# Performance work log

Hardware: AMD Instinct MI355X
Metric: run time of the kernel (lower is better)

## Reference

```python
import jax, jax.numpy as jnp
import numpy as np

N = 50000      # nodes
E = 800000     # edges (before self-loops)
IN = 256       # in_channels
HID = 16       # hidden_channels per head
HEADS = 8
OUT = 64       # out_channels (classes)
NEG_SLOPE = 0.2  # PyG GATConv leaky_relu slope


def setup_inputs() -> dict:
    key = jax.random.key(0)
    ks = jax.random.split(key, 10)
    x = jax.random.normal(ks[0], (N, IN), jnp.float32)
    edge_index = jax.random.randint(ks[1], (2, E), 0, N, dtype=jnp.int32)
    g = lambda k, shape: jax.random.normal(k, shape, jnp.float32) * (1.0 / np.sqrt(shape[0]))
    W1 = g(ks[2], (IN, HEADS * HID))
    a_src1 = jax.random.normal(ks[3], (HEADS, HID), jnp.float32) * 0.1
    a_dst1 = jax.random.normal(ks[4], (HEADS, HID), jnp.float32) * 0.1
    b1 = jnp.zeros((HEADS * HID,), jnp.float32)
    W2 = g(ks[5], (HEADS * HID, OUT))
    a_src2 = jax.random.normal(ks[6], (1, OUT), jnp.float32) * 0.1
    a_dst2 = jax.random.normal(ks[7], (1, OUT), jnp.float32) * 0.1
    b2 = jnp.zeros((OUT,), jnp.float32)
    return {"x": x, "edge_index": edge_index, "W1": W1, "a_src1": a_src1,
            "a_dst1": a_dst1, "b1": b1, "W2": W2, "a_src2": a_src2,
            "a_dst2": a_dst2, "b2": b2}


def gat_conv(x, src, dst, W, a_s, a_d, b, heads, concat):
    # x: [n, f]; edges src->dst; attention softmax over incoming edges of dst
    n = x.shape[0]
    h = (x @ W).reshape(n, heads, -1)                 # [n, H, d]
    al_s = jnp.einsum('nhd,hd->nh', h, a_s)           # [n, H]
    al_d = jnp.einsum('nhd,hd->nh', h, a_d)
    e = jax.nn.leaky_relu(al_s[src] + al_d[dst], negative_slope=NEG_SLOPE)  # [E, H]
    m = jax.ops.segment_max(e, dst, num_segments=n)   # stable scatter-softmax
    ex = jnp.exp(e - m[dst])
    den = jax.ops.segment_sum(ex, dst, num_segments=n)
    alpha = ex / (den[dst] + 1e-16)                   # [E, H]
    out = jax.ops.segment_sum(h[src] * alpha[:, :, None], dst, num_segments=n)  # [n, H, d]
    out = out.reshape(n, -1) if concat else out.mean(axis=1)
    return out + b


def reference(x, edge_index, W1, a_src1, a_dst1, b1, W2, a_src2, a_dst2, b2):
    # inference mode: dropout disabled. PyG GATConv adds self-loops by default.
    n = x.shape[0]
    loop = jnp.arange(n, dtype=edge_index.dtype)
    ei = jnp.concatenate([edge_index, jnp.stack([loop, loop])], axis=1)
    src, dst = ei[0], ei[1]
    h = gat_conv(x, src, dst, W1, a_src1, a_dst1, b1, HEADS, True)
    h = jax.nn.elu(h)
    h = gat_conv(h, src, dst, W2, a_src2, a_dst2, b2, 1, False)
    return jax.nn.log_softmax(h, axis=1)
```

## Files before the change

kernel.cpp:

```cpp
#include <hip/hip_runtime.h>
#include <hip/hip_bf16.h>


typedef __attribute__((ext_vector_type(8))) short short8;
typedef __attribute__((ext_vector_type(4))) float f4;
typedef __attribute__((ext_vector_type(2))) float float2v;

#define NCHUNK 64
#define NRANGE 4
#define RSIZE 16384
#define CONVB 80

#define A1PAD 72
#define B1PAD 264
#define G2PAD 136

__device__ __forceinline__ unsigned short f2bf(float f) {
  unsigned int u = __builtin_bit_cast(unsigned int, f);
  u += 0x7fffu + ((u >> 16) & 1u);
  return (unsigned short)(u >> 16);
}
__device__ __forceinline__ float bf2f(unsigned short h) {
  unsigned int u = ((unsigned int)h) << 16;
  return __builtin_bit_cast(float, u);
}

__device__ __forceinline__ unsigned char f2fp8(float f) {
  unsigned int u = __builtin_bit_cast(unsigned int, f);
  unsigned int s = (u >> 24) & 0x80u;
  float a = fabsf(f);
  a = fminf(a, 448.f);
  if (a < 0.015625f) {
    int m = (int)rintf(a * 512.f);
    return (unsigned char)(s | (unsigned)m);
  }
  unsigned int ub = __builtin_bit_cast(unsigned int, a);
  ub += 0xFFFFFu + ((ub >> 20) & 1u);
  unsigned int e = (ub >> 23) - 120u;
  unsigned int m = (ub >> 20) & 7u;
  if (e > 15u) { e = 15u; m = 6u; }
  return (unsigned char)(s | (e << 3) | m);
}

__global__ __launch_bounds__(512) void hist_kernel(const int* __restrict__ ei,
                                                   int* __restrict__ hist,
                                                   const float* __restrict__ W1,
                                                   const float* __restrict__ W2,
                                                   unsigned short* __restrict__ Wt1,
                                                   unsigned short* __restrict__ Wt2,
                                                   int E, int N, int ET, int CS) {
  if (blockIdx.x >= NCHUNK * NRANGE) {
    int i = (blockIdx.x - NCHUNK * NRANGE) * 512 + threadIdx.x;
    if (i < 128 * 256) {
      int n = i >> 8, k = i & 255;
      Wt1[i] = f2bf(W1[k * 128 + n]);
    } else {
      int j = i - 128 * 256;
      if (j < 64 * 128) {
        int n = j >> 7, k = j & 127;
        Wt2[j] = f2bf(W2[k * 64 + n]);
      }
    }
    return;
  }
  __shared__ int lh[RSIZE];
  const int c = blockIdx.x & (NCHUNK - 1);
  const int r = blockIdx.x >> 6;
  const int base = r * RSIZE;
  for (int i = threadIdx.x; i < RSIZE; i += 512) lh[i] = 0;
  __syncthreads();
  const int e0 = c * CS, e1 = min(e0 + CS, ET);
  for (int e = e0 + threadIdx.x; e < e1; e += 512) {
    int d = (e < E) ? ei[E + e] : (e - E);
    unsigned dl = (unsigned)(d - base);
    if (dl < RSIZE) atomicAdd(&lh[dl], 1);
  }
  __syncthreads();
  for (int i = threadIdx.x; i < RSIZE; i += 512) {
    int d = base + i;
    if (d < N) hist[c * N + d] = lh[i];
  }
}

__global__ __launch_bounds__(256) void colscan_kernel(int* __restrict__ hist,
                                                      int* __restrict__ deg, int N) {
  int d = blockIdx.x * 256 + threadIdx.x;
  if (d >= N) return;
  int run = 0;
#pragma unroll 8
  for (int c = 0; c < NCHUNK; ++c) {
    int v = hist[c * N + d];
    hist[c * N + d] = run;
    run += v;
  }
  deg[d] = run;
}

__global__ __launch_bounds__(1024) void scan1_kernel(const int* __restrict__ deg,
                                                     int* __restrict__ rowptr,
                                                     int* __restrict__ bsum, int N) {
  __shared__ int wtot[16];
  const int lane = threadIdx.x & 63, wid = threadIdx.x >> 6;
  int i = blockIdx.x * 1024 + threadIdx.x;
  int v = (i < N) ? deg[i] : 0;
  int incl = v;
#pragma unroll
  for (int off = 1; off < 64; off <<= 1) {
    int t = __shfl_up(incl, off, 64);
    if (lane >= off) incl += t;
  }
  if (lane == 63) wtot[wid] = incl;
  __syncthreads();
  int woff = 0;
#pragma unroll
  for (int w = 0; w < 16; ++w) woff += (w < wid) ? wtot[w] : 0;
  if (i < N) rowptr[i] = woff + incl - v;
  if (threadIdx.x == 1023) bsum[blockIdx.x] = woff + incl;
}

__global__ __launch_bounds__(256) void scan3_kernel(int* __restrict__ rowptr,
                                                    const int* __restrict__ bsum,
                                                    int N, int ET) {
  int lane = threadIdx.x & 63;
  int g = blockIdx.x >> 2;
  int bv = (lane < g) ? bsum[lane] : 0;
#pragma unroll
  for (int off = 32; off; off >>= 1) bv += __shfl_xor(bv, off, 64);
  int i = blockIdx.x * 256 + threadIdx.x;
  if (i < N) rowptr[i] += bv;
  if (i == N) rowptr[N] = ET;
}

__global__ __launch_bounds__(512) void scatter2_kernel(const int* __restrict__ ei,
                                                       const int* __restrict__ hist,
                                                       const int* __restrict__ rowptr,
                                                       int* __restrict__ csr_src,
                                                       int E, int N, int ET, int CS) {
  __shared__ int lh[RSIZE];
  const int c = blockIdx.x & (NCHUNK - 1);
  const int r = blockIdx.x >> 6;
  const int base = r * RSIZE;
  for (int i = threadIdx.x; i < RSIZE; i += 512) {
    int d = base + i;
    lh[i] = (d < N) ? (rowptr[d] + hist[c * N + d]) : 0;
  }
  __syncthreads();
  const int e0 = c * CS, e1 = min(e0 + CS, ET);
  for (int e = e0 + threadIdx.x; e < e1; e += 512) {
    int s, d;
    if (e < E) { s = ei[e]; d = ei[E + e]; }
    else       { s = e - E; d = s; }
    unsigned dl = (unsigned)(d - base);
    if (dl < RSIZE) {
      int slot = atomicAdd(&lh[dl], 1);
      csr_src[slot] = s;
    }
  }
}

__global__ __launch_bounds__(256) void gemm1_mfma(const float* __restrict__ X,
                                                  const unsigned short* __restrict__ Wt,
                                                  const float* __restrict__ as1,
                                                  const float* __restrict__ ad1,
                                                  unsigned char* __restrict__ H,
                                                  float* __restrict__ als,
                                                  float* __restrict__ ald,
                                                  int M) {
  __shared__ unsigned short Bs[64 * B1PAD];
  __shared__ unsigned short As[2][64 * A1PAD];
  const int t = threadIdx.x;
  const int ln = t & 63;
  const int wv = t >> 6;
  const int ml = ln & 15, q = ln >> 4;
  const int ch = blockIdx.x & 1;
  const int rb = (blockIdx.x >> 1) * 64;
  const int r0 = rb + wv * 16;
  const int alr = wv * 16 + ml;

  int srow[4], skg[4];
#pragma unroll
  for (int i = 0; i < 4; ++i) {
    int g = i * 256 + t;
    srow[i] = g >> 4;
    skg[i] = g & 15;
  }

  float4 astg[4];
#pragma unroll
  for (int i = 0; i < 4; ++i)
    astg[i] = *(const float4*)(X + (size_t)min(rb + srow[i], M - 1) * 256 + skg[i] * 4);

#pragma unroll
  for (int i = 0; i < 8; ++i) {
    int g = i * 256 + t;
    int brow = g >> 5, bc = g & 31;
    *(short8*)&Bs[brow * B1PAD + bc * 8] =
        *(const short8*)(Wt + (size_t)(ch * 64 + brow) * 256 + bc * 8);
  }

#pragma unroll
  for (int i = 0; i < 4; ++i) {
    ushort4 pk;
    pk.x = f2bf(astg[i].x); pk.y = f2bf(astg[i].y);
    pk.z = f2bf(astg[i].z); pk.w = f2bf(astg[i].w);
    *(ushort4*)&As[0][srow[i] * A1PAD + skg[i] * 4] = pk;
  }
  __syncthreads();

  f4 acc[4];
#pragma unroll
  for (int b = 0; b < 4; ++b) acc[b] = (f4)0.f;

#pragma unroll
  for (int s = 0; s < 4; ++s) {
    const int buf = s & 1;
    if (s < 3) {
#pragma unroll
      for (int i = 0; i < 4; ++i)
        astg[i] = *(const float4*)(X + (size_t)min(rb + srow[i], M - 1) * 256 +
                                   (s + 1) * 64 + skg[i] * 4);
    }
#pragma unroll
    for (int kk = 0; kk < 2; ++kk) {
      short8 av = *(const short8*)&As[buf][alr * A1PAD + kk * 32 + q * 8];
#pragma unroll
      for (int b = 0; b < 4; ++b) {
        short8 bfr = *(const short8*)&Bs[(b * 16 + ml) * B1PAD + s * 64 + kk * 32 + q * 8];
        acc[b] = __builtin_amdgcn_mfma_f32_16x16x32_bf16(av, bfr, acc[b], 0, 0, 0);
      }
    }
    if (s < 3) {
#pragma unroll
      for (int i = 0; i < 4; ++i) {
        ushort4 pk;
        pk.x = f2bf(astg[i].x); pk.y = f2bf(astg[i].y);
        pk.z = f2bf(astg[i].z); pk.w = f2bf(astg[i].w);
        *(ushort4*)&As[buf ^ 1][srow[i] * A1PAD + skg[i] * 4] = pk;
      }
    }
    __syncthreads();
  }

#pragma unroll
  for (int i = 0; i < 4; ++i) {
    int rr = r0 + q * 4 + i;
    bool ok = rr < M;
    if (ok) {
#pragma unroll
      for (int b = 0; b < 4; ++b)
        H[(size_t)rr * 128 + ch * 64 + b * 16 + ml] = f2fp8(acc[b][i]);
    }
#pragma unroll
    for (int b = 0; b < 4; ++b) {
      float ps = acc[b][i] * as1[ch * 64 + b * 16 + ml];
      float pd = acc[b][i] * ad1[ch * 64 + b * 16 + ml];
#pragma unroll
      for (int off = 1; off < 16; off <<= 1) {
        ps += __shfl_xor(ps, off, 16);
        pd += __shfl_xor(pd, off, 16);
      }
      if (ok && ml == b) {
        als[(size_t)rr * 8 + ch * 4 + b] = ps;
        ald[(size_t)rr * 8 + ch * 4 + b] = pd;
      }
    }
  }
}

__global__ __launch_bounds__(256) void gemm2_mfma(const unsigned short* __restrict__ Xb,
                                                  const unsigned short* __restrict__ Wt,
                                                  const float* __restrict__ as2,
                                                  const float* __restrict__ ad2,
                                                  unsigned char* __restrict__ H,
                                                  float* __restrict__ als,
                                                  float* __restrict__ ald,
                                                  int M) {
  __shared__ unsigned short Asl[64 * G2PAD];
  __shared__ unsigned short Bsl[64 * G2PAD];
  const int t = threadIdx.x;
  const int ln = t & 63;
  const int wv = t >> 6;
  const int ml = ln & 15, q = ln >> 4;
  const int rb = blockIdx.x * 64;
  const int r0 = rb + wv * 16;
  const int alr = wv * 16 + ml;

#pragma unroll
  for (int i = 0; i < 4; ++i) {
    int g = i * 256 + t;
    int row = g >> 4, kg = g & 15;
    *(short8*)&Asl[row * G2PAD + kg * 8] =
        *(const short8*)(Xb + (size_t)min(rb + row, M - 1) * 128 + kg * 8);
    *(short8*)&Bsl[row * G2PAD + kg * 8] =
        *(const short8*)(Wt + (size_t)row * 128 + kg * 8);
  }
  __syncthreads();

  short8 av[4];
#pragma unroll
  for (int s = 0; s < 4; ++s)
    av[s] = *(const short8*)&Asl[alr * G2PAD + s * 32 + q * 8];

  f4 acc[4];
#pragma unroll
  for (int b = 0; b < 4; ++b) acc[b] = (f4)0.f;

#pragma unroll
  for (int s = 0; s < 4; ++s) {
#pragma unroll
    for (int b = 0; b < 4; ++b) {
      short8 bfr = *(const short8*)&Bsl[(b * 16 + ml) * G2PAD + s * 32 + q * 8];
      acc[b] = __builtin_amdgcn_mfma_f32_16x16x32_bf16(av[s], bfr, acc[b], 0, 0, 0);
    }
  }

#pragma unroll
  for (int i = 0; i < 4; ++i) {
    int rr = r0 + q * 4 + i;
    bool ok = rr < M;
    if (ok) {
#pragma unroll
      for (int b = 0; b < 4; ++b)
        H[(size_t)rr * 64 + b * 16 + ml] = f2fp8(acc[b][i]);
    }
    float ps = 0.f, pd = 0.f;
#pragma unroll
    for (int b = 0; b < 4; ++b) {
      ps += acc[b][i] * as2[b * 16 + ml];
      pd += acc[b][i] * ad2[b * 16 + ml];
    }
#pragma unroll
    for (int off = 1; off < 16; off <<= 1) {
      ps += __shfl_xor(ps, off, 16);
      pd += __shfl_xor(pd, off, 16);
    }
    if (ok && ml == 0) { als[rr] = ps; ald[rr] = pd; }
  }
}

__global__ __launch_bounds__(256) void attn1_kernel(
    const unsigned char* __restrict__ h1, const float* __restrict__ als,
    const float* __restrict__ ald, const float* __restrict__ b1,
    const int* __restrict__ rowptr, const int* __restrict__ csr_src,
    unsigned short* __restrict__ helu, int N) {
  int d = __builtin_amdgcn_readfirstlane(
      (blockIdx.x * blockDim.x + threadIdx.x) >> 6);
  int lane = threadIdx.x & 63;
  if (d >= N) return;
  const int hh = lane >> 3;
  const int hw = lane & 7;
  const int ew = lane >> 3;
  const float aldp = ald[d * 8 + hw];
  const int beg = rowptr[d], end = rowptr[d + 1];
  const unsigned char* h1l = h1 + 2 * lane;
  float den = 0.f, ax = 0.f, ay = 0.f;

  for (int p0 = beg; p0 < end; p0 += 8) {
    int idx = p0 + ew;
    int se = csr_src[idx < end ? idx : end - 1];
    float v = als[se * 8 + hw] + aldp;
    v = fmaxf(v, 0.2f * v);
    float w = (idx < end) ? __expf(v) : 0.f;
#pragma unroll
    for (int j = 0; j < 4; ++j) {
      float wj = __shfl(w, j * 8 + hh);
      int sj = __shfl(se, j * 8);
      unsigned short pk = *(const unsigned short*)(h1l + (size_t)sj * 128);
      float2v g = __builtin_amdgcn_cvt_pk_f32_fp8(pk, false);
      den += wj; ax += wj * g.x; ay += wj * g.y;
    }
    if (p0 + 4 < end) {
#pragma unroll
      for (int j = 4; j < 8; ++j) {
        float wj = __shfl(w, j * 8 + hh);
        int sj = __shfl(se, j * 8);
        unsigned short pk = *(const unsigned short*)(h1l + (size_t)sj * 128);
        float2v g = __builtin_amdgcn_cvt_pk_f32_fp8(pk, false);
        den += wj; ax += wj * g.x; ay += wj * g.y;
      }
    }
  }

  float inv = 1.0f / (den + 1e-16f);
  float2 bb = *(const float2*)(b1 + 2 * lane);
  float o0 = ax * inv + bb.x;
  float o1 = ay * inv + bb.y;
  o0 = o0 > 0.f ? o0 : __expf(o0) - 1.0f;
  o1 = o1 > 0.f ? o1 : __expf(o1) - 1.0f;
  ushort2 ov; ov.x = f2bf(o0); ov.y = f2bf(o1);
  *(ushort2*)(helu + (size_t)d * 128 + 2 * lane) = ov;
}

__global__ __launch_bounds__(256) void attn2_kernel(
    const unsigned char* __restrict__ h2, const float* __restrict__ als,
    const float* __restrict__ ald, const float* __restrict__ b2,
    const int* __restrict__ rowptr, const int* __restrict__ csr_src,
    float* __restrict__ out, int N) {
  int d = __builtin_amdgcn_readfirstlane(
      (blockIdx.x * blockDim.x + threadIdx.x) >> 6);
  int lane = threadIdx.x & 63;
  if (d >= N) return;
  const float aldd = ald[d];
  const int beg = rowptr[d], end = rowptr[d + 1];
  const unsigned char* h2l = h2 + lane;
  float den = 0.f, acc = 0.f;

  for (int p0 = beg; p0 < end; p0 += 64) {
    int idx = p0 + lane;
    int se = csr_src[idx < end ? idx : end - 1];
    float v = als[se] + aldd;
    v = fmaxf(v, 0.2f * v);
    float w = (idx < end) ? __expf(v) : 0.f;
    int cnt = min(64, end - p0);
    for (int j0 = 0; j0 < cnt; j0 += 4) {
#pragma unroll
      for (int j = 0; j < 4; ++j) {
        float wj = __shfl(w, j0 + j);
        int sj = __shfl(se, j0 + j);
        float g = __builtin_amdgcn_cvt_f32_fp8(h2l[(size_t)sj * 64], 0);
        den += wj; acc += wj * g;
      }
    }
  }

  float z = acc / (den + 1e-16f) + b2[lane];
  float zm = z;
#pragma unroll
  for (int off = 32; off; off >>= 1) zm = fmaxf(zm, __shfl_xor(zm, off, 64));
  float ex = __expf(z - zm), se2 = ex;
#pragma unroll
  for (int off = 32; off; off >>= 1) se2 += __shfl_xor(se2, off, 64);
  out[(size_t)d * 64 + lane] = z - zm - __logf(se2);
}

extern "C" void kernel_launch(void* const* d_in, const int* in_sizes, int n_in,
                              void* d_out, int out_size, void* d_ws, size_t ws_size,
                              hipStream_t stream) {
  const int N = in_sizes[0] / 256;
  const int E = in_sizes[1] / 2;
  const int ET = E + N;
  const int CS = (ET + NCHUNK - 1) / NCHUNK;
  const int NB = (N + 1023) / 1024;

  const float* x   = (const float*)d_in[0];
  const int*   ei  = (const int*)d_in[1];
  const float* W1  = (const float*)d_in[2];
  const float* as1 = (const float*)d_in[3];
  const float* ad1 = (const float*)d_in[4];
  const float* b1  = (const float*)d_in[5];
  const float* W2  = (const float*)d_in[6];
  const float* as2 = (const float*)d_in[7];
  const float* ad2 = (const float*)d_in[8];
  const float* b2  = (const float*)d_in[9];
  float* out = (float*)d_out;

  char* p = (char*)d_ws;
  unsigned char* h1f8 = (unsigned char*)p; p += (size_t)N * 128;
  unsigned char* h2f8 = h1f8;
  unsigned short* helu = (unsigned short*)p; p += (size_t)NCHUNK * N * 4;
  int* hist = (int*)helu;
  unsigned short* Wt1  = (unsigned short*)p; p += (size_t)128 * 256 * 2;
  unsigned short* Wt2  = (unsigned short*)p; p += (size_t)64 * 128 * 2;
  float* als1 = (float*)p; p += (size_t)N * 8 * 4;
  float* ald1 = (float*)p; p += (size_t)N * 8 * 4;
  float* als2 = (float*)p; p += (size_t)N * 4;
  float* ald2 = (float*)p; p += (size_t)N * 4;
  int* deg     = (int*)p; p += (size_t)N * 4;
  int* rowptr  = (int*)p; p += (size_t)(N + 1) * 4;
  int* bsum    = (int*)p; p += 64 * 4;
  int* csr_src = (int*)p; p += (size_t)ET * 4;

  hist_kernel<<<NCHUNK * NRANGE + CONVB, 512, 0, stream>>>(ei, hist, W1, W2, Wt1, Wt2,
                                                           E, N, ET, CS);
  colscan_kernel<<<(N + 255) / 256, 256, 0, stream>>>(hist, deg, N);
  scan1_kernel<<<NB, 1024, 0, stream>>>(deg, rowptr, bsum, N);
  scan3_kernel<<<(N + 256) / 256, 256, 0, stream>>>(rowptr, bsum, N, ET);
  scatter2_kernel<<<NCHUNK * NRANGE, 512, 0, stream>>>(ei, hist, rowptr, csr_src, E, N, ET, CS);

  gemm1_mfma<<<2 * ((N + 63) / 64), 256, 0, stream>>>(x, Wt1, as1, ad1, h1f8, als1, ald1, N);
  attn1_kernel<<<(N + 3) / 4, 256, 0, stream>>>(h1f8, als1, ald1, b1, rowptr, csr_src, helu, N);

  gemm2_mfma<<<(N + 63) / 64, 256, 0, stream>>>(helu, Wt2, as2, ad2, h2f8, als2, ald2, N);
  attn2_kernel<<<(N + 3) / 4, 256, 0, stream>>>(h2f8, als2, ald2, b2, rowptr, csr_src, out, N);
}
```

Before: 253.9 us.

## Replace chunked LDS histogram CSR build with global atomic counting and scatter

The multi-chunk shared-memory histogram, column scan and chunked scatter are replaced by a global atomicAdd degree count (self-loops preset to 1) and a scatter that atomically bumps rowptr to claim slots. After the scatter, rowptr[d] holds the end of row d, so the attention kernels read the row start from rowptr[d-1]. This drops the 64xN histogram traffic and the colscan kernel. The cost is contended global atomics and a non-deterministic order of edges within each row, which changes the floating-point summation order.

```diff
diff --git a/kernel.cpp b/kernel.cpp
--- a/kernel.cpp
+++ b/kernel.cpp
@@ -6,9 +6,6 @@
 typedef __attribute__((ext_vector_type(4))) float f4;
 typedef __attribute__((ext_vector_type(2))) float float2v;
 
-#define NCHUNK 64
-#define NRANGE 4
-#define RSIZE 16384
 #define CONVB 80
 
 #define A1PAD 72
@@ -42,15 +39,14 @@
   return (unsigned char)(s | (e << 3) | m);
 }
 
-__global__ __launch_bounds__(512) void hist_kernel(const int* __restrict__ ei,
-                                                   int* __restrict__ hist,
-                                                   const float* __restrict__ W1,
-                                                   const float* __restrict__ W2,
-                                                   unsigned short* __restrict__ Wt1,
-                                                   unsigned short* __restrict__ Wt2,
-                                                   int E, int N, int ET, int CS) {
-  if (blockIdx.x >= NCHUNK * NRANGE) {
-    int i = (blockIdx.x - NCHUNK * NRANGE) * 512 + threadIdx.x;
+__global__ __launch_bounds__(512) void zerodeg_kernel(int* __restrict__ deg,
+                                                      const float* __restrict__ W1,
+                                                      const float* __restrict__ W2,
+                                                      unsigned short* __restrict__ Wt1,
+                                                      unsigned short* __restrict__ Wt2,
+                                                      int N, int ZB) {
+  if (blockIdx.x >= (unsigned)ZB) {
+    int i = (blockIdx.x - ZB) * 512 + threadIdx.x;
     if (i < 128 * 256) {
       int n = i >> 8, k = i & 255;
       Wt1[i] = f2bf(W1[k * 128 + n]);
@@ -63,37 +59,17 @@
     }
     return;
   }
-  __shared__ int lh[RSIZE];
-  const int c = blockIdx.x & (NCHUNK - 1);
-  const int r = blockIdx.x >> 6;
-  const int base = r * RSIZE;
-  for (int i = threadIdx.x; i < RSIZE; i += 512) lh[i] = 0;
-  __syncthreads();
-  const int e0 = c * CS, e1 = min(e0 + CS, ET);
-  for (int e = e0 + threadIdx.x; e < e1; e += 512) {
-    int d = (e < E) ? ei[E + e] : (e - E);
-    unsigned dl = (unsigned)(d - base);
-    if (dl < RSIZE) atomicAdd(&lh[dl], 1);
-  }
-  __syncthreads();
-  for (int i = threadIdx.x; i < RSIZE; i += 512) {
-    int d = base + i;
-    if (d < N) hist[c * N + d] = lh[i];
-  }
-}
-
-__global__ __launch_bounds__(256) void colscan_kernel(int* __restrict__ hist,
-                                                      int* __restrict__ deg, int N) {
-  int d = blockIdx.x * 256 + threadIdx.x;
-  if (d >= N) return;
-  int run = 0;
-#pragma unroll 8
-  for (int c = 0; c < NCHUNK; ++c) {
-    int v = hist[c * N + d];
-    hist[c * N + d] = run;
-    run += v;
-  }
-  deg[d] = run;
+  int i = blockIdx.x * 512 + threadIdx.x;
+  if (i < N) deg[i] = 1;
+}
+
+__global__ __launch_bounds__(512) void degcnt_kernel(const int* __restrict__ ei,
+                                                     int* __restrict__ deg, int E) {
+  int stride = gridDim.x * 512;
+  for (int e = blockIdx.x * 512 + threadIdx.x; e < E; e += stride) {
+    int d = ei[E + e];
+    atomicAdd(&deg[d], 1);
+  }
 }
 
 __global__ __launch_bounds__(1024) void scan1_kernel(const int* __restrict__ deg,
@@ -131,30 +107,17 @@
   if (i == N) rowptr[N] = ET;
 }
 
-__global__ __launch_bounds__(512) void scatter2_kernel(const int* __restrict__ ei,
-                                                       const int* __restrict__ hist,
-                                                       const int* __restrict__ rowptr,
-                                                       int* __restrict__ csr_src,
-                                                       int E, int N, int ET, int CS) {
-  __shared__ int lh[RSIZE];
-  const int c = blockIdx.x & (NCHUNK - 1);
-  const int r = blockIdx.x >> 6;
-  const int base = r * RSIZE;
-  for (int i = threadIdx.x; i < RSIZE; i += 512) {
-    int d = base + i;
-    lh[i] = (d < N) ? (rowptr[d] + hist[c * N + d]) : 0;
-  }
-  __syncthreads();
-  const int e0 = c * CS, e1 = min(e0 + CS, ET);
-  for (int e = e0 + threadIdx.x; e < e1; e += 512) {
+__global__ __launch_bounds__(512) void scatter_kernel(const int* __restrict__ ei,
+                                                      int* __restrict__ rowptr,
+                                                      int* __restrict__ csr_src,
+                                                      int E, int ET) {
+  int stride = gridDim.x * 512;
+  for (int e = blockIdx.x * 512 + threadIdx.x; e < ET; e += stride) {
     int s, d;
     if (e < E) { s = ei[e]; d = ei[E + e]; }
     else       { s = e - E; d = s; }
-    unsigned dl = (unsigned)(d - base);
-    if (dl < RSIZE) {
-      int slot = atomicAdd(&lh[dl], 1);
-      csr_src[slot] = s;
-    }
+    int slot = atomicAdd(&rowptr[d], 1);
+    csr_src[slot] = s;
   }
 }
 
@@ -351,7 +314,7 @@
   const int hw = lane & 7;
   const int ew = lane >> 3;
   const float aldp = ald[d * 8 + hw];
-  const int beg = rowptr[d], end = rowptr[d + 1];
+  const int beg = d ? rowptr[d - 1] : 0, end = rowptr[d];
   const unsigned char* h1l = h1 + 2 * lane;
   float den = 0.f, ax = 0.f, ay = 0.f;
 
@@ -401,7 +364,7 @@
   int lane = threadIdx.x & 63;
   if (d >= N) return;
   const float aldd = ald[d];
-  const int beg = rowptr[d], end = rowptr[d + 1];
+  const int beg = d ? rowptr[d - 1] : 0, end = rowptr[d];
   const unsigned char* h2l = h2 + lane;
   float den = 0.f, acc = 0.f;
 
@@ -439,8 +402,8 @@
   const int N = in_sizes[0] / 256;
   const int E = in_sizes[1] / 2;
   const int ET = E + N;
-  const int CS = (ET + NCHUNK - 1) / NCHUNK;
   const int NB = (N + 1023) / 1024;
+  const int ZB = (N + 511) / 512;
 
   const float* x   = (const float*)d_in[0];
   const int*   ei  = (const int*)d_in[1];
@@ -457,8 +420,7 @@
   char* p = (char*)d_ws;
   unsigned char* h1f8 = (unsigned char*)p; p += (size_t)N * 128;
   unsigned char* h2f8 = h1f8;
-  unsigned short* helu = (unsigned short*)p; p += (size_t)NCHUNK * N * 4;
-  int* hist = (int*)helu;
+  unsigned short* helu = (unsigned short*)p; p += (size_t)N * 128 * 2;
   unsigned short* Wt1  = (unsigned short*)p; p += (size_t)128 * 256 * 2;
   unsigned short* Wt2  = (unsigned short*)p; p += (size_t)64 * 128 * 2;
   float* als1 = (float*)p; p += (size_t)N * 8 * 4;
@@ -470,12 +432,11 @@
   int* bsum    = (int*)p; p += 64 * 4;
   int* csr_src = (int*)p; p += (size_t)ET * 4;
 
-  hist_kernel<<<NCHUNK * NRANGE + CONVB, 512, 0, stream>>>(ei, hist, W1, W2, Wt1, Wt2,
-                                                           E, N, ET, CS);
-  colscan_kernel<<<(N + 255) / 256, 256, 0, stream>>>(hist, deg, N);
+  zerodeg_kernel<<<ZB + CONVB, 512, 0, stream>>>(deg, W1, W2, Wt1, Wt2, N, ZB);
+  degcnt_kernel<<<400, 512, 0, stream>>>(ei, deg, E);
   scan1_kernel<<<NB, 1024, 0, stream>>>(deg, rowptr, bsum, N);
   scan3_kernel<<<(N + 256) / 256, 256, 0, stream>>>(rowptr, bsum, N, ET);
-  scatter2_kernel<<<NCHUNK * NRANGE, 512, 0, stream>>>(ei, hist, rowptr, csr_src, E, N, ET, CS);
+  scatter_kernel<<<420, 512, 0, stream>>>(ei, rowptr, csr_src, E, ET);
 
   gemm1_mfma<<<2 * ((N + 63) / 64), 256, 0, stream>>>(x, Wt1, as1, ad1, h1f8, als1, ald1, N);
   attn1_kernel<<<(N + 3) / 4, 256, 0, stream>>>(h1f8, als1, ald1, b1, rowptr, csr_src, helu, N);
```

New measurement: 295.9 us. 16.5% more time.
